# Optimization experiments

Measured on AMD Instinct MI355X. Metric: run time of the kernel, lower is better.

Reference implementation:

```python
import jax, jax.numpy as jnp
import numpy as np

N = 50000
E = 600000
IN_C = 128
OUT_C = 64
HID = 2 * OUT_C  # 128


def setup_inputs() -> dict:
    key = jax.random.key(0)
    ks = jax.random.split(key, 8)
    x = jax.random.normal(ks[0], (N, IN_C), dtype=jnp.float32)
    edge_index = jax.random.randint(ks[1], (2, E), 0, N, dtype=jnp.int64)
    # Glorot-style init for GCN weights, zero bias (PyG default)
    def glorot(k, fan_in, fan_out):
        s = jnp.sqrt(6.0 / (fan_in + fan_out)).astype(jnp.float32)
        return jax.random.uniform(k, (fan_in, fan_out), jnp.float32, -s, s)
    return {
        "x": x,
        "edge_index": edge_index,
        "W1": glorot(ks[2], IN_C, HID),
        "b1": jnp.zeros((HID,), jnp.float32),
        "W_mu": glorot(ks[3], HID, OUT_C),
        "b_mu": jnp.zeros((OUT_C,), jnp.float32),
        "W_ls": glorot(ks[4], HID, OUT_C),
        "b_ls": jnp.zeros((OUT_C,), jnp.float32),
    }


def _gcn_norm(edge_index, num_nodes):
    # Add self-loops, compute symmetric normalization (cached=True in original
    # means this is computed once and reused by all three convs -- same math).
    loop = jnp.arange(num_nodes, dtype=edge_index.dtype)
    row = jnp.concatenate([edge_index[0], loop])  # source
    col = jnp.concatenate([edge_index[1], loop])  # target
    deg = jax.ops.segment_sum(jnp.ones_like(col, dtype=jnp.float32), col,
                              num_segments=num_nodes)
    dis = jnp.where(deg > 0, jax.lax.rsqrt(deg), 0.0)  # deg^{-1/2}, inf->0
    norm = dis[row] * dis[col]  # [E+N]
    return row, col, norm


def _gcn_conv(x, W, b, row, col, norm, num_nodes):
    h = x @ W                                  # dense transform [N, out]
    msg = h[row] * norm[:, None]               # gather + scale [E+N, out]
    out = jax.ops.segment_sum(msg, col, num_segments=num_nodes)
    return out + b


def reference(x, edge_index, W1, b1, W_mu, b_mu, W_ls, b_ls):
    num_nodes = x.shape[0]
    row, col, norm = _gcn_norm(edge_index, num_nodes)
    # eval mode: F.dropout is identity when not training
    h = jax.nn.relu(_gcn_conv(x, W1, b1, row, col, norm, num_nodes))
    mu = _gcn_conv(h, W_mu, b_mu, row, col, norm, num_nodes)
    logstd = _gcn_conv(h, W_ls, b_ls, row, col, norm, num_nodes)
    return mu, logstd
```

## Files before the change

kernel.cpp:

```cpp
#include <hip/hip_runtime.h>
#include <hip/hip_fp16.h>


#define N_NODES 50000
#define N_EDGES 600000
#define MU_SIZE (N_NODES * 64)
#define SCAN_BLOCKS 200
#define SCAN_CHUNK 250
#define WT_S 136

typedef _Float16 half8 __attribute__((ext_vector_type(8)));
typedef _Float16 half4 __attribute__((ext_vector_type(4)));
typedef float floatx4 __attribute__((ext_vector_type(4)));

union H8 { __half2 h2[4]; float4 f4; };

__global__ __launch_bounds__(256) void prep_zero_kernel(const float* __restrict__ W1,
                                                        const float* __restrict__ Wmu,
                                                        const float* __restrict__ Wls,
                                                        _Float16* __restrict__ W1T,
                                                        _Float16* __restrict__ W2T,
                                                        int* __restrict__ zero_base) {
  int idx = blockIdx.x * 256 + threadIdx.x;
  for (int i = idx; i < 2 * N_NODES; i += 32768) zero_base[i] = 0;
  int e = idx & 16383;
  int n = e >> 7, k = e & 127;
  if (idx < 16384) {
    W1T[e] = (_Float16)W1[k * 128 + n];
  } else {
    float w = (n < 64) ? Wmu[k * 64 + n] : Wls[k * 64 + (n - 64)];
    W2T[e] = (_Float16)w;
  }
}

__global__ __launch_bounds__(256) void count_kernel(const int* __restrict__ col,
                                                    int* __restrict__ counts, int e) {
  int i = blockIdx.x * 256 + threadIdx.x;
  if (i < e) atomicAdd(&counts[col[i]], 1);
}

__global__ __launch_bounds__(256) void blocksum_dis_kernel(const int* __restrict__ counts,
                                                           float* __restrict__ dis,
                                                           int* __restrict__ blocksums) {
  __shared__ int red[4];
  int b = blockIdx.x, t = threadIdx.x;
  int i = b * SCAN_CHUNK + t;
  int c = 0;
  if (t < SCAN_CHUNK) {
    c = counts[i];
    dis[i] = rsqrtf((float)(c + 1));
  }
  int s = c;
#pragma unroll
  for (int off = 32; off > 0; off >>= 1) s += __shfl_down(s, off, 64);
  if ((t & 63) == 0) red[t >> 6] = s;
  __syncthreads();
  if (t == 0) blocksums[b] = red[0] + red[1] + red[2] + red[3];
}

__global__ __launch_bounds__(256) void offsets_kernel(const int* __restrict__ counts,
                                                      const int* __restrict__ blocksums,
                                                      int* __restrict__ offsets) {
  __shared__ int sb[256];
  __shared__ int loc[256];
  int b = blockIdx.x, t = threadIdx.x;
  sb[t] = (t < SCAN_BLOCKS) ? blocksums[t] : 0;
  __syncthreads();
#pragma unroll
  for (int off = 1; off < 256; off <<= 1) {
    int v = (t >= off) ? sb[t - off] : 0;
    __syncthreads();
    sb[t] += v;
    __syncthreads();
  }
  int base = (b == 0) ? 0 : sb[b - 1];
  int i = b * SCAN_CHUNK + t;
  int c = (t < SCAN_CHUNK) ? counts[i] : 0;
  loc[t] = c;
  __syncthreads();
#pragma unroll
  for (int off = 1; off < 256; off <<= 1) {
    int v = (t >= off) ? loc[t - off] : 0;
    __syncthreads();
    loc[t] += v;
    __syncthreads();
  }
  if (t < SCAN_CHUNK) offsets[i] = base + loc[t] - c;
  if (b == SCAN_BLOCKS - 1 && t == SCAN_CHUNK - 1) offsets[N_NODES] = base + loc[t];
}

__global__ __launch_bounds__(256) void fill_kernel(const int* __restrict__ row,
                                                   const int* __restrict__ col,
                                                   const int* __restrict__ offsets,
                                                   int* __restrict__ fillcnt,
                                                   int* __restrict__ srcidx, int e) {
  int i = blockIdx.x * 256 + threadIdx.x;
  if (i < e) {
    int c = col[i];
    int pos = offsets[c] + atomicAdd(&fillcnt[c], 1);
    srcidx[pos] = row[i];
  }
}

template <bool SPLIT>
__global__ __launch_bounds__(256) void gemm_mfma_kernel(const float* __restrict__ X,
                                                        const _Float16* __restrict__ Xh,
                                                        const _Float16* __restrict__ WT,
                                                        const float* __restrict__ dis,
                                                        const float* __restrict__ ba,
                                                        const float* __restrict__ bb,
                                                        _Float16* __restrict__ Yh,
                                                        float* __restrict__ Yf) {
  __shared__ _Float16 WL[128 * WT_S];

  int t = threadIdx.x;
  for (int idx = t; idx < 128 * 16; idx += 256) {
    int n = idx >> 4, kk = (idx & 15) * 8;
    *(half8*)&WL[n * WT_S + kk] = *(const half8*)&WT[n * 128 + kk];
  }
  __syncthreads();

  int wid = t >> 6, lane = t & 63;
  int q = lane >> 4, m = lane & 15;

  int node = blockIdx.x * 64 + wid * 16 + m;
  size_t nr = (size_t)min(node, N_NODES - 1);
  bool valid = node < N_NODES;

  half8 xfrag[4];
  if (!SPLIT) {
#pragma unroll
    for (int c = 0; c < 4; ++c) {
      const float* ap = &X[nr * 128 + 32 * c + 8 * q];
      float4 a0 = *(const float4*)ap;
      float4 a1 = *(const float4*)(ap + 4);
      half8 af = {(_Float16)a0.x, (_Float16)a0.y, (_Float16)a0.z, (_Float16)a0.w,
                  (_Float16)a1.x, (_Float16)a1.y, (_Float16)a1.z, (_Float16)a1.w};
      xfrag[c] = af;
    }
  } else {
#pragma unroll
    for (int c = 0; c < 4; ++c) {
      xfrag[c] = *(const half8*)&Xh[nr * 128 + 32 * c + 8 * q];
    }
  }
  float dnode = SPLIT ? 0.f : dis[nr];

#pragma unroll
  for (int f = 0; f < 8; ++f) {
    floatx4 acc = {0.f, 0.f, 0.f, 0.f};
#pragma unroll
    for (int c = 0; c < 4; ++c) {
      half8 wfrag = *(const half8*)&WL[(16 * f + m) * WT_S + 32 * c + 8 * q];
      acc = __builtin_amdgcn_mfma_f32_16x16x32_f16(wfrag, xfrag[c], acc, 0, 0, 0);
    }
    int fbase = 16 * f + 4 * q;
    if (!SPLIT) {
      if (valid) {
        half4 o = {(_Float16)(acc[0] * dnode), (_Float16)(acc[1] * dnode),
                   (_Float16)(acc[2] * dnode), (_Float16)(acc[3] * dnode)};
        *(half4*)&Yh[(size_t)node * 128 + fbase] = o;
      }
    } else {
      float4 bias = (f < 4) ? *(const float4*)&ba[fbase]
                            : *(const float4*)&bb[fbase - 64];
      float4 o = make_float4(acc[0] + bias.x, acc[1] + bias.y, acc[2] + bias.z,
                             acc[3] + bias.w);
      if (valid) {
        if (f < 4)
          *(float4*)&Yf[(size_t)node * 64 + fbase] = o;
        else
          *(float4*)&Yf[MU_SIZE + (size_t)node * 64 + (fbase - 64)] = o;
      }
    }
  }
}

template <bool BIAS_RELU>
__global__ __launch_bounds__(256) void aggregate_kernel(const __half* __restrict__ Hs,
                                                        const int* __restrict__ offsets,
                                                        const int* __restrict__ srcidx,
                                                        const float* __restrict__ dis,
                                                        const float* __restrict__ bias,
                                                        __half* __restrict__ outH, int n) {
  int wid = threadIdx.x >> 6, lane = threadIdx.x & 63;
  int q = lane >> 4, ql = lane & 15;
  int i = blockIdx.x * 16 + wid * 4 + q;
  if (i >= n) return;
  float di = dis[i];
  float4 selfv = ((const float4*)(Hs + (size_t)i * 128))[ql];
  float acc[8] = {0.f, 0.f, 0.f, 0.f, 0.f, 0.f, 0.f, 0.f};
  int k = offsets[i], end = offsets[i + 1];
  for (; k + 7 < end; k += 8) {
    int r[8];
#pragma unroll
    for (int u = 0; u < 8; ++u) r[u] = srcidx[k + u];
    float4 v[8];
#pragma unroll
    for (int u = 0; u < 8; ++u) v[u] = ((const float4*)(Hs + (size_t)r[u] * 128))[ql];
#pragma unroll
    for (int u = 0; u < 8; ++u) {
      const __half2* a = (const __half2*)&v[u];
#pragma unroll
      for (int j = 0; j < 4; ++j) {
        float2 f = __half22float2(a[j]);
        acc[2 * j] += f.x;
        acc[2 * j + 1] += f.y;
      }
    }
  }
  for (; k + 3 < end; k += 4) {
    int r[4];
#pragma unroll
    for (int u = 0; u < 4; ++u) r[u] = srcidx[k + u];
    float4 v[4];
#pragma unroll
    for (int u = 0; u < 4; ++u) v[u] = ((const float4*)(Hs + (size_t)r[u] * 128))[ql];
#pragma unroll
    for (int u = 0; u < 4; ++u) {
      const __half2* a = (const __half2*)&v[u];
#pragma unroll
      for (int j = 0; j < 4; ++j) {
        float2 f = __half22float2(a[j]);
        acc[2 * j] += f.x;
        acc[2 * j + 1] += f.y;
      }
    }
  }
  for (; k < end; ++k) {
    int r0 = srcidx[k];
    float4 v0 = ((const float4*)(Hs + (size_t)r0 * 128))[ql];
    const __half2* a0 = (const __half2*)&v0;
#pragma unroll
    for (int j = 0; j < 4; ++j) {
      float2 f0 = __half22float2(a0[j]);
      acc[2 * j] += f0.x;
      acc[2 * j + 1] += f0.y;
    }
  }
  const __half2* sh = (const __half2*)&selfv;
  float s[8];
#pragma unroll
  for (int j = 0; j < 4; ++j) {
    float2 f = __half22float2(sh[j]);
    s[2 * j] = di * (acc[2 * j] + f.x);
    s[2 * j + 1] = di * (acc[2 * j + 1] + f.y);
  }
  H8 u;
  if (BIAS_RELU) {
    float4 b0 = ((const float4*)bias)[2 * ql];
    float4 b1 = ((const float4*)bias)[2 * ql + 1];
    u.h2[0] = __float22half2_rn(
        make_float2(di * fmaxf(s[0] + b0.x, 0.f), di * fmaxf(s[1] + b0.y, 0.f)));
    u.h2[1] = __float22half2_rn(
        make_float2(di * fmaxf(s[2] + b0.z, 0.f), di * fmaxf(s[3] + b0.w, 0.f)));
    u.h2[2] = __float22half2_rn(
        make_float2(di * fmaxf(s[4] + b1.x, 0.f), di * fmaxf(s[5] + b1.y, 0.f)));
    u.h2[3] = __float22half2_rn(
        make_float2(di * fmaxf(s[6] + b1.z, 0.f), di * fmaxf(s[7] + b1.w, 0.f)));
  } else {
    u.h2[0] = __float22half2_rn(make_float2(s[0], s[1]));
    u.h2[1] = __float22half2_rn(make_float2(s[2], s[3]));
    u.h2[2] = __float22half2_rn(make_float2(s[4], s[5]));
    u.h2[3] = __float22half2_rn(make_float2(s[6], s[7]));
  }
  ((float4*)(outH + (size_t)i * 128))[ql] = u.f4;
}

extern "C" void kernel_launch(void* const* d_in, const int* in_sizes, int n_in,
                              void* d_out, int out_size, void* d_ws, size_t ws_size,
                              hipStream_t stream) {
  const float* x = (const float*)d_in[0];
  const int* ei = (const int*)d_in[1];
  const float* W1 = (const float*)d_in[2];
  const float* b1 = (const float*)d_in[3];
  const float* Wmu = (const float*)d_in[4];
  const float* bmu = (const float*)d_in[5];
  const float* Wls = (const float*)d_in[6];
  const float* bls = (const float*)d_in[7];
  float* out = (float*)d_out;

  const int* row = ei;
  const int* col = ei + N_EDGES;

  __half* bufAh = (__half*)d_ws;
  __half* bufBh = bufAh + 6400000;
  __half* bufCh = bufBh + 6400000;
  float* dis = (float*)(bufCh + 6400000);
  int* counts = (int*)(dis + N_NODES);
  int* fillcnt = counts + N_NODES;
  int* offsets = fillcnt + N_NODES;
  int* srcidx = offsets + N_NODES + 1;
  int* blocksums = srcidx + N_EDGES;
  _Float16* W1T = (_Float16*)(blocksums + 256);
  _Float16* W2T = W1T + 16384;

  prep_zero_kernel<<<128, 256, 0, stream>>>(W1, Wmu, Wls, W1T, W2T, counts);

  int eb = (N_EDGES + 255) / 256;
  count_kernel<<<eb, 256, 0, stream>>>(col, counts, N_EDGES);
  blocksum_dis_kernel<<<SCAN_BLOCKS, 256, 0, stream>>>(counts, dis, blocksums);
  offsets_kernel<<<SCAN_BLOCKS, 256, 0, stream>>>(counts, blocksums, offsets);
  fill_kernel<<<eb, 256, 0, stream>>>(row, col, offsets, fillcnt, srcidx, N_EDGES);

  int gb = (N_NODES + 63) / 64;
  gemm_mfma_kernel<false><<<gb, 256, 0, stream>>>(x, nullptr, W1T, dis, nullptr, nullptr,
                                                  (_Float16*)bufAh, nullptr);
  int ab = (N_NODES + 15) / 16;
  aggregate_kernel<true><<<ab, 256, 0, stream>>>(bufAh, offsets, srcidx, dis, b1,
                                                 bufBh, N_NODES);
  aggregate_kernel<false><<<ab, 256, 0, stream>>>(bufBh, offsets, srcidx, dis,
                                                  nullptr, bufCh, N_NODES);
  gemm_mfma_kernel<true><<<gb, 256, 0, stream>>>(nullptr, (const _Float16*)bufCh, W2T,
                                                 nullptr, bmu, bls, nullptr, out);
}
```

Before: 223.3 us.

## Fuse second aggregation with output GEMM through shared-memory staging

Merges the second neighbor aggregation and the final mu/logstd GEMM into one kernel. Each block aggregates 64 nodes into a shared-memory tile, then runs the MFMA transform directly from it. This removes one kernel launch and the round-trip of the intermediate fp16 buffer through global memory. In exchange, each block holds 64 nodes (16 threads per node, 4 nodes per thread sequentially), which reduces parallelism in the gather phase and raises shared-memory use per block, possibly lowering occupancy.

After: 231.7 us. +3.8%, slower.

```diff
diff --git a/kernel.cpp b/kernel.cpp
--- a/kernel.cpp
+++ b/kernel.cpp
@@ -102,15 +102,10 @@
   }
 }
 
-template <bool SPLIT>
-__global__ __launch_bounds__(256) void gemm_mfma_kernel(const float* __restrict__ X,
-                                                        const _Float16* __restrict__ Xh,
-                                                        const _Float16* __restrict__ WT,
-                                                        const float* __restrict__ dis,
-                                                        const float* __restrict__ ba,
-                                                        const float* __restrict__ bb,
-                                                        _Float16* __restrict__ Yh,
-                                                        float* __restrict__ Yf) {
+__global__ __launch_bounds__(256) void gemm1_mfma_kernel(const float* __restrict__ X,
+                                                         const _Float16* __restrict__ WT,
+                                                         const float* __restrict__ dis,
+                                                         _Float16* __restrict__ Yh) {
   __shared__ _Float16 WL[128 * WT_S];
 
   int t = threadIdx.x;
@@ -128,23 +123,16 @@
   bool valid = node < N_NODES;
 
   half8 xfrag[4];
-  if (!SPLIT) {
-#pragma unroll
-    for (int c = 0; c < 4; ++c) {
-      const float* ap = &X[nr * 128 + 32 * c + 8 * q];
-      float4 a0 = *(const float4*)ap;
-      float4 a1 = *(const float4*)(ap + 4);
-      half8 af = {(_Float16)a0.x, (_Float16)a0.y, (_Float16)a0.z, (_Float16)a0.w,
-                  (_Float16)a1.x, (_Float16)a1.y, (_Float16)a1.z, (_Float16)a1.w};
-      xfrag[c] = af;
-    }
-  } else {
-#pragma unroll
-    for (int c = 0; c < 4; ++c) {
-      xfrag[c] = *(const half8*)&Xh[nr * 128 + 32 * c + 8 * q];
-    }
-  }
-  float dnode = SPLIT ? 0.f : dis[nr];
+#pragma unroll
+  for (int c = 0; c < 4; ++c) {
+    const float* ap = &X[nr * 128 + 32 * c + 8 * q];
+    float4 a0 = *(const float4*)ap;
+    float4 a1 = *(const float4*)(ap + 4);
+    half8 af = {(_Float16)a0.x, (_Float16)a0.y, (_Float16)a0.z, (_Float16)a0.w,
+                (_Float16)a1.x, (_Float16)a1.y, (_Float16)a1.z, (_Float16)a1.w};
+    xfrag[c] = af;
+  }
+  float dnode = dis[nr];
 
 #pragma unroll
   for (int f = 0; f < 8; ++f) {
@@ -155,34 +143,20 @@
       acc = __builtin_amdgcn_mfma_f32_16x16x32_f16(wfrag, xfrag[c], acc, 0, 0, 0);
     }
     int fbase = 16 * f + 4 * q;
-    if (!SPLIT) {
-      if (valid) {
-        half4 o = {(_Float16)(acc[0] * dnode), (_Float16)(acc[1] * dnode),
-                   (_Float16)(acc[2] * dnode), (_Float16)(acc[3] * dnode)};
-        *(half4*)&Yh[(size_t)node * 128 + fbase] = o;
-      }
-    } else {
-      float4 bias = (f < 4) ? *(const float4*)&ba[fbase]
-                            : *(const float4*)&bb[fbase - 64];
-      float4 o = make_float4(acc[0] + bias.x, acc[1] + bias.y, acc[2] + bias.z,
-                             acc[3] + bias.w);
-      if (valid) {
-        if (f < 4)
-          *(float4*)&Yf[(size_t)node * 64 + fbase] = o;
-        else
-          *(float4*)&Yf[MU_SIZE + (size_t)node * 64 + (fbase - 64)] = o;
-      }
-    }
-  }
-}
-
-template <bool BIAS_RELU>
-__global__ __launch_bounds__(256) void aggregate_kernel(const __half* __restrict__ Hs,
-                                                        const int* __restrict__ offsets,
-                                                        const int* __restrict__ srcidx,
-                                                        const float* __restrict__ dis,
-                                                        const float* __restrict__ bias,
-                                                        __half* __restrict__ outH, int n) {
+    if (valid) {
+      half4 o = {(_Float16)(acc[0] * dnode), (_Float16)(acc[1] * dnode),
+                 (_Float16)(acc[2] * dnode), (_Float16)(acc[3] * dnode)};
+      *(half4*)&Yh[(size_t)node * 128 + fbase] = o;
+    }
+  }
+}
+
+__global__ __launch_bounds__(256) void aggregate1_kernel(const __half* __restrict__ Hs,
+                                                         const int* __restrict__ offsets,
+                                                         const int* __restrict__ srcidx,
+                                                         const float* __restrict__ dis,
+                                                         const float* __restrict__ bias,
+                                                         __half* __restrict__ outH, int n) {
   int wid = threadIdx.x >> 6, lane = threadIdx.x & 63;
   int q = lane >> 4, ql = lane & 15;
   int i = blockIdx.x * 16 + wid * 4 + q;
@@ -246,25 +220,144 @@
     s[2 * j] = di * (acc[2 * j] + f.x);
     s[2 * j + 1] = di * (acc[2 * j + 1] + f.y);
   }
+  float4 b0 = ((const float4*)bias)[2 * ql];
+  float4 b1 = ((const float4*)bias)[2 * ql + 1];
   H8 u;
-  if (BIAS_RELU) {
-    float4 b0 = ((const float4*)bias)[2 * ql];
-    float4 b1 = ((const float4*)bias)[2 * ql + 1];
-    u.h2[0] = __float22half2_rn(
-        make_float2(di * fmaxf(s[0] + b0.x, 0.f), di * fmaxf(s[1] + b0.y, 0.f)));
-    u.h2[1] = __float22half2_rn(
-        make_float2(di * fmaxf(s[2] + b0.z, 0.f), di * fmaxf(s[3] + b0.w, 0.f)));
-    u.h2[2] = __float22half2_rn(
-        make_float2(di * fmaxf(s[4] + b1.x, 0.f), di * fmaxf(s[5] + b1.y, 0.f)));
-    u.h2[3] = __float22half2_rn(
-        make_float2(di * fmaxf(s[6] + b1.z, 0.f), di * fmaxf(s[7] + b1.w, 0.f)));
-  } else {
-    u.h2[0] = __float22half2_rn(make_float2(s[0], s[1]));
-    u.h2[1] = __float22half2_rn(make_float2(s[2], s[3]));
-    u.h2[2] = __float22half2_rn(make_float2(s[4], s[5]));
-    u.h2[3] = __float22half2_rn(make_float2(s[6], s[7]));
-  }
+  u.h2[0] = __float22half2_rn(
+      make_float2(di * fmaxf(s[0] + b0.x, 0.f), di * fmaxf(s[1] + b0.y, 0.f)));
+  u.h2[1] = __float22half2_rn(
+      make_float2(di * fmaxf(s[2] + b0.z, 0.f), di * fmaxf(s[3] + b0.w, 0.f)));
+  u.h2[2] = __float22half2_rn(
+      make_float2(di * fmaxf(s[4] + b1.x, 0.f), di * fmaxf(s[5] + b1.y, 0.f)));
+  u.h2[3] = __float22half2_rn(
+      make_float2(di * fmaxf(s[6] + b1.z, 0.f), di * fmaxf(s[7] + b1.w, 0.f)));
   ((float4*)(outH + (size_t)i * 128))[ql] = u.f4;
+}
+
+__global__ __launch_bounds__(256) void agg2_gemm2_kernel(const __half* __restrict__ Hs,
+                                                         const int* __restrict__ offsets,
+                                                         const int* __restrict__ srcidx,
+                                                         const float* __restrict__ dis,
+                                                         const _Float16* __restrict__ W2T,
+                                                         const float* __restrict__ bmu,
+                                                         const float* __restrict__ bls,
+                                                         float* __restrict__ out) {
+  __shared__ _Float16 WL[128 * WT_S];
+  __shared__ _Float16 ZL[64 * WT_S];
+
+  int t = threadIdx.x;
+  for (int idx = t; idx < 128 * 16; idx += 256) {
+    int n = idx >> 4, kk = (idx & 15) * 8;
+    *(half8*)&WL[n * WT_S + kk] = *(const half8*)&W2T[n * 128 + kk];
+  }
+
+  int qw = t >> 4, ql = t & 15;
+  int base = blockIdx.x * 64;
+#pragma unroll
+  for (int it = 0; it < 4; ++it) {
+    int nl = qw * 4 + it;
+    int i = base + nl;
+    H8 u;
+    if (i < N_NODES) {
+      float di = dis[i];
+      float4 selfv = ((const float4*)(Hs + (size_t)i * 128))[ql];
+      float acc[8] = {0.f, 0.f, 0.f, 0.f, 0.f, 0.f, 0.f, 0.f};
+      int k = offsets[i], end = offsets[i + 1];
+      for (; k + 7 < end; k += 8) {
+        int r[8];
+#pragma unroll
+        for (int u8 = 0; u8 < 8; ++u8) r[u8] = srcidx[k + u8];
+        float4 v[8];
+#pragma unroll
+        for (int u8 = 0; u8 < 8; ++u8)
+          v[u8] = ((const float4*)(Hs + (size_t)r[u8] * 128))[ql];
+#pragma unroll
+        for (int u8 = 0; u8 < 8; ++u8) {
+          const __half2* a = (const __half2*)&v[u8];
+#pragma unroll
+          for (int j = 0; j < 4; ++j) {
+            float2 f = __half22float2(a[j]);
+            acc[2 * j] += f.x;
+            acc[2 * j + 1] += f.y;
+          }
+        }
+      }
+      for (; k + 3 < end; k += 4) {
+        int r[4];
+#pragma unroll
+        for (int u4 = 0; u4 < 4; ++u4) r[u4] = srcidx[k + u4];
+        float4 v[4];
+#pragma unroll
+        for (int u4 = 0; u4 < 4; ++u4)
+          v[u4] = ((const float4*)(Hs + (size_t)r[u4] * 128))[ql];
+#pragma unroll
+        for (int u4 = 0; u4 < 4; ++u4) {
+          const __half2* a = (const __half2*)&v[u4];
+#pragma unroll
+          for (int j = 0; j < 4; ++j) {
+            float2 f = __half22float2(a[j]);
+            acc[2 * j] += f.x;
+            acc[2 * j + 1] += f.y;
+          }
+        }
+      }
+      for (; k < end; ++k) {
+        int r0 = srcidx[k];
+        float4 v0 = ((const float4*)(Hs + (size_t)r0 * 128))[ql];
+        const __half2* a0 = (const __half2*)&v0;
+#pragma unroll
+        for (int j = 0; j < 4; ++j) {
+          float2 f0 = __half22float2(a0[j]);
+          acc[2 * j] += f0.x;
+          acc[2 * j + 1] += f0.y;
+        }
+      }
+      const __half2* sh = (const __half2*)&selfv;
+#pragma unroll
+      for (int j = 0; j < 4; ++j) {
+        float2 f = __half22float2(sh[j]);
+        u.h2[j] = __float22half2_rn(make_float2(di * (acc[2 * j] + f.x),
+                                                di * (acc[2 * j + 1] + f.y)));
+      }
+    } else {
+      u.f4 = make_float4(0.f, 0.f, 0.f, 0.f);
+    }
+    *(float4*)&ZL[nl * WT_S + ql * 8] = u.f4;
+  }
+  __syncthreads();
+
+  int wid = t >> 6, lane = t & 63;
+  int q = lane >> 4, m = lane & 15;
+  int nl = wid * 16 + m;
+  int node = base + nl;
+  bool valid = node < N_NODES;
+
+  half8 zfrag[4];
+#pragma unroll
+  for (int c = 0; c < 4; ++c) {
+    zfrag[c] = *(const half8*)&ZL[nl * WT_S + 32 * c + 8 * q];
+  }
+
+#pragma unroll
+  for (int f = 0; f < 8; ++f) {
+    floatx4 acc = {0.f, 0.f, 0.f, 0.f};
+#pragma unroll
+    for (int c = 0; c < 4; ++c) {
+      half8 wfrag = *(const half8*)&WL[(16 * f + m) * WT_S + 32 * c + 8 * q];
+      acc = __builtin_amdgcn_mfma_f32_16x16x32_f16(wfrag, zfrag[c], acc, 0, 0, 0);
+    }
+    int fbase = 16 * f + 4 * q;
+    float4 bias = (f < 4) ? *(const float4*)&bmu[fbase]
+                          : *(const float4*)&bls[fbase - 64];
+    float4 o = make_float4(acc[0] + bias.x, acc[1] + bias.y, acc[2] + bias.z,
+                           acc[3] + bias.w);
+    if (valid) {
+      if (f < 4)
+        *(float4*)&out[(size_t)node * 64 + fbase] = o;
+      else
+        *(float4*)&out[MU_SIZE + (size_t)node * 64 + (fbase - 64)] = o;
+    }
+  }
 }
 
 extern "C" void kernel_launch(void* const* d_in, const int* in_sizes, int n_in,
@@ -285,8 +378,7 @@
 
   __half* bufAh = (__half*)d_ws;
   __half* bufBh = bufAh + 6400000;
-  __half* bufCh = bufBh + 6400000;
-  float* dis = (float*)(bufCh + 6400000);
+  float* dis = (float*)(bufBh + 6400000);
   int* counts = (int*)(dis + N_NODES);
   int* fillcnt = counts + N_NODES;
   int* offsets = fillcnt + N_NODES;
@@ -304,13 +396,10 @@
   fill_kernel<<<eb, 256, 0, stream>>>(row, col, offsets, fillcnt, srcidx, N_EDGES);
 
   int gb = (N_NODES + 63) / 64;
-  gemm_mfma_kernel<false><<<gb, 256, 0, stream>>>(x, nullptr, W1T, dis, nullptr, nullptr,
-                                                  (_Float16*)bufAh, nullptr);
+  gemm1_mfma_kernel<<<gb, 256, 0, stream>>>(x, W1T, dis, (_Float16*)bufAh);
   int ab = (N_NODES + 15) / 16;
-  aggregate_kernel<true><<<ab, 256, 0, stream>>>(bufAh, offsets, srcidx, dis, b1,
-                                                 bufBh, N_NODES);
-  aggregate_kernel<false><<<ab, 256, 0, stream>>>(bufBh, offsets, srcidx, dis,
-                                                  nullptr, bufCh, N_NODES);
-  gemm_mfma_kernel<true><<<gb, 256, 0, stream>>>(nullptr, (const _Float16*)bufCh, W2T,
-                                                 nullptr, bmu, bls, nullptr, out);
-}
+  aggregate1_kernel<<<ab, 256, 0, stream>>>(bufAh, offsets, srcidx, dis, b1,
+                                            bufBh, N_NODES);
+  agg2_gemm2_kernel<<<gb, 256, 0, stream>>>(bufBh, offsets, srcidx, dis, W2T,
+                                            bmu, bls, out);
+}
```
